# Performance work log

Measured on AMD Instinct MI355X. Metric: run time of the kernel, lower is better.

## Reference

```python
import jax, jax.numpy as jnp
import numpy as np

DIM = 1024
HEADS = 16
DH = DIM // HEADS          # 64
SEQ_LEN = 4096
LATENT = 1024
HIST = SEQ_LEN - LATENT    # 3072
LN_EPS = 1e-5


def setup_inputs() -> dict:
    key = jax.random.key(0)
    ks = jax.random.split(key, 5)
    b = 2
    x = jax.random.normal(ks[0], (b, SEQ_LEN, DIM), dtype=jnp.float32)
    s = 0.02
    Wq = jax.random.normal(ks[1], (DIM, DIM), dtype=jnp.float32) * s
    Wkv = jax.random.normal(ks[2], (DIM, DIM), dtype=jnp.float32) * s
    Wo = jax.random.normal(ks[3], (DIM, DIM), dtype=jnp.float32) * s
    bo = jnp.zeros((DIM,), dtype=jnp.float32)
    gamma = jnp.ones((DH,), dtype=jnp.float32)
    beta = jnp.zeros((DH,), dtype=jnp.float32)
    return {"x": x, "Wq": Wq, "Wkv": Wkv, "Wo": Wo, "bo": bo,
            "gamma": gamma, "beta": beta}


def _rotate_half(t):
    t1, t2 = jnp.split(t, 2, axis=-1)
    return jnp.concatenate([-t2, t1], axis=-1)


def reference(x, Wq, Wkv, Wo, bo, gamma, beta):
    b, n, dim = x.shape
    # projections (nn.Linear: y = x @ W.T), split heads -> (b, h, n, d)
    q = jnp.einsum('bnd,ed->bne', x, Wq).reshape(b, n, HEADS, DH).transpose(0, 2, 1, 3)
    kv = jnp.einsum('bnd,ed->bne', x, Wkv).reshape(b, n, HEADS, DH).transpose(0, 2, 1, 3)

    # layer_num == 0: queries only for the latent segment
    q = q[:, :, HIST:, :]  # (b, h, latent, d)

    # rotary embeddings: concat-style freqs over head dim
    inv_freq = 1.0 / (10000.0 ** (jnp.arange(0, DH, 2, dtype=jnp.float32) / DH))
    freqs = jnp.arange(n, dtype=jnp.float32)[:, None] * inv_freq[None, :]  # (n, DH/2)
    emb = jnp.concatenate([freqs, freqs], axis=-1)  # (n, DH)
    cos, sin = jnp.cos(emb), jnp.sin(emb)
    q = q * cos[HIST:] + _rotate_half(q) * sin[HIST:]
    kv = kv * cos + _rotate_half(kv) * sin

    q = q * (DH ** -0.5)

    # per-kv LayerNorm over head dim
    mu = kv.mean(axis=-1, keepdims=True)
    var = ((kv - mu) ** 2).mean(axis=-1, keepdims=True)
    kvn = (kv - mu) * jax.lax.rsqrt(var + LN_EPS) * gamma + beta

    attn = jnp.einsum('bhid,bhjd->bhij', q, kvn)  # (b, h, latent, n)

    # causal mask only on latent columns: col j (>= HIST) masked if j-HIST > i
    i = jnp.arange(LATENT)[:, None]
    j = jnp.arange(n)[None, :]
    mask = (j - HIST) > i  # false for history columns (j < HIST)
    neg = -jnp.finfo(attn.dtype).max
    attn = jnp.where(mask, neg, attn)

    attn = jax.nn.softmax(attn, axis=-1)
    out = jnp.einsum('bhij,bhjd->bhid', attn, kvn)  # (b, h, latent, d)
    out = out.transpose(0, 2, 1, 3).reshape(b, LATENT, dim)
    return jnp.einsum('bnd,ed->bne', out, Wo) + bo
```

## Files before the change

### kernel.cpp

```cpp
#include <hip/hip_runtime.h>
#include <hip/hip_bf16.h>
#include <cstdint>

#define DIMC 1024
#define HEADS 16
#define DHH 64
#define SEQ 4096
#define LATENT 1024
#define HISTC 3072
#define BATCH 2

typedef __attribute__((ext_vector_type(8))) __bf16 bf16x8;
typedef __attribute__((ext_vector_type(4))) float f32x4;
typedef __attribute__((ext_vector_type(16))) float f32x16;

__global__ void k_convert(const float* __restrict__ in, __bf16* __restrict__ out, int n) {
  int stride = gridDim.x * blockDim.x;
  int nc = n >> 2;
  for (int i = blockIdx.x * blockDim.x + threadIdx.x; i < nc; i += stride) {
    float4 v = reinterpret_cast<const float4*>(in)[i];
    union { __bf16 h[4]; uint64_t u; } p;
    p.h[0] = (__bf16)v.x; p.h[1] = (__bf16)v.y;
    p.h[2] = (__bf16)v.z; p.h[3] = (__bf16)v.w;
    reinterpret_cast<uint64_t*>(out)[i] = p.u;
  }
}

__global__ void k_convert3(const float* __restrict__ a, const float* __restrict__ b,
                           const float* __restrict__ c, __bf16* __restrict__ oa,
                           __bf16* __restrict__ ob, __bf16* __restrict__ oc) {
  int id = blockIdx.x;
  const float* src; __bf16* dst;
  if (id < 512) { src = a; dst = oa; }
  else if (id < 1024) { src = b; dst = ob; id -= 512; }
  else { src = c; dst = oc; id -= 1024; }
#pragma unroll
  for (int k = 0; k < 2; ++k) {
    int idx = id * 512 + k * 256 + threadIdx.x;
    float4 v = reinterpret_cast<const float4*>(src)[idx];
    union { __bf16 h[4]; uint64_t u; } p;
    p.h[0] = (__bf16)v.x; p.h[1] = (__bf16)v.y;
    p.h[2] = (__bf16)v.z; p.h[3] = (__bf16)v.w;
    reinterpret_cast<uint64_t*>(dst)[idx] = p.u;
  }
}

__device__ __forceinline__ void gload16(void* lds, const void* g) {
  __builtin_amdgcn_global_load_lds(
      (const __attribute__((address_space(1))) unsigned int*)g,
      (__attribute__((address_space(3))) unsigned int*)lds, 16, 0, 0);
}

template<int QREMAP, int BIAS>
__launch_bounds__(256)
__global__ void k_gemm(const __bf16* __restrict__ A, const __bf16* __restrict__ Bw,
                       float* __restrict__ C, const float* __restrict__ bias,
                       int M, int N, int K) {
  __shared__ __align__(16) char lds[16384];
  const int t = threadIdx.x;
  const int l = t & 63, w = t >> 6;
  const int wr = w >> 1, wc = w & 1;
  const int m0 = blockIdx.y * 128, n0 = blockIdx.x * 128;
  const int lrow = l & 15, lk = l >> 4;
  f32x4 acc[4][4] = {};

  for (int k0 = 0; k0 < K; k0 += 32) {
    if (k0) __syncthreads();
#pragma unroll
    for (int i = 0; i < 2; ++i) {
      int c = i * 256 + t;
      int row = c >> 2, kc = c & 3;
      int mi = m0 + row;
      if (QREMAP) mi += HISTC + (mi >> 10) * HISTC;
      gload16(lds + c * 16, A + (size_t)mi * K + k0 + kc * 8);
      gload16(lds + 8192 + c * 16, Bw + (size_t)(n0 + row) * K + k0 + kc * 8);
    }
    __syncthreads();
    bf16x8 af[4], bfr[4];
#pragma unroll
    for (int m = 0; m < 4; ++m)
      af[m] = *reinterpret_cast<const bf16x8*>(lds + (wr * 64 + m * 16 + lrow) * 64 + lk * 16);
#pragma unroll
    for (int n = 0; n < 4; ++n)
      bfr[n] = *reinterpret_cast<const bf16x8*>(lds + 8192 + (wc * 64 + n * 16 + lrow) * 64 + lk * 16);
#pragma unroll
    for (int m = 0; m < 4; ++m)
#pragma unroll
      for (int n = 0; n < 4; ++n)
        acc[m][n] = __builtin_amdgcn_mfma_f32_16x16x32_bf16(af[m], bfr[n], acc[m][n], 0, 0, 0);
  }

#pragma unroll
  for (int m = 0; m < 4; ++m)
#pragma unroll
    for (int n = 0; n < 4; ++n)
#pragma unroll
      for (int r = 0; r < 4; ++r) {
        int row = m0 + wr * 64 + m * 16 + (l >> 4) * 4 + r;
        int col = n0 + wc * 64 + n * 16 + (l & 15);
        float v = acc[m][n][r];
        if (BIAS) v += bias[col];
        C[(size_t)row * N + col] = v;
      }
}

__launch_bounds__(256)
__global__ void k_gemmqkv(const __bf16* __restrict__ x16,
                          const __bf16* __restrict__ wkv16,
                          const __bf16* __restrict__ wq16,
                          __bf16* __restrict__ kvn, __bf16* __restrict__ kvnT,
                          __bf16* __restrict__ qb,
                          const float* __restrict__ gamma,
                          const float* __restrict__ beta) {
  __shared__ __align__(16) char lds[16384];
  const int t = threadIdx.x, l = t & 63, w = t >> 6;
  const int wr = w >> 1, wc = w & 1;
  const int by = blockIdx.y;
  const bool isq = by >= 64;
  const int m0 = (isq ? (by - 64) : by) * 128;
  const int n0 = blockIdx.x * 128;
  const __bf16* Bw = isq ? wq16 : wkv16;
  const int lrow = l & 15, lk = l >> 4;
  f32x4 acc[4][4] = {};

  for (int k0 = 0; k0 < 1024; k0 += 32) {
    if (k0) __syncthreads();
#pragma unroll
    for (int i = 0; i < 2; ++i) {
      int c = i * 256 + t;
      int row = c >> 2, kc = c & 3;
      int mi = m0 + row;
      if (isq) mi += HISTC + (mi >> 10) * HISTC;
      gload16(lds + c * 16, x16 + (size_t)mi * 1024 + k0 + kc * 8);
      gload16(lds + 8192 + c * 16, Bw + (size_t)(n0 + row) * 1024 + k0 + kc * 8);
    }
    __syncthreads();
    bf16x8 af[4], bfr[4];
#pragma unroll
    for (int m = 0; m < 4; ++m)
      af[m] = *reinterpret_cast<const bf16x8*>(lds + (wr * 64 + m * 16 + lrow) * 64 + lk * 16);
#pragma unroll
    for (int n = 0; n < 4; ++n)
      bfr[n] = *reinterpret_cast<const bf16x8*>(lds + 8192 + (wc * 64 + n * 16 + lrow) * 64 + lk * 16);
#pragma unroll
    for (int m = 0; m < 4; ++m)
#pragma unroll
      for (int n = 0; n < 4; ++n)
        acc[m][n] = __builtin_amdgcn_mfma_f32_16x16x32_bf16(af[m], bfr[n], acc[m][n], 0, 0, 0);
  }

  const float LG = 0.41524101186f;
  float invf0 = exp2f(-(float)lrow * LG);
  float invf1 = exp2f(-(float)(lrow + 16) * LG);
#pragma unroll
  for (int m = 0; m < 4; ++m)
#pragma unroll
    for (int r = 0; r < 4; ++r) {
      int rl = wr * 64 + m * 16 + lk * 4 + r;
      int pos = isq ? (HISTC + ((m0 + rl) & 1023)) : ((m0 + rl) & 4095);
      float fp = (float)pos;
      float s0, c0, s1, c1;
      sincosf(fp * invf0, &s0, &c0);
      sincosf(fp * invf1, &s1, &c1);
      float a0 = acc[m][0][r], a2 = acc[m][2][r];
      acc[m][0][r] = a0 * c0 - a2 * s0;
      acc[m][2][r] = a2 * c0 + a0 * s0;
      float a1 = acc[m][1][r], a3 = acc[m][3][r];
      acc[m][1][r] = a1 * c1 - a3 * s1;
      acc[m][3][r] = a3 * c1 + a1 * s1;
    }

  const int h = (n0 + wc * 64) >> 6;
  if (!isq) {
    float g4[4], b4[4];
#pragma unroll
    for (int n = 0; n < 4; ++n) { g4[n] = gamma[n * 16 + lrow]; b4[n] = beta[n * 16 + lrow]; }
#pragma unroll
    for (int m = 0; m < 4; ++m)
#pragma unroll
      for (int r = 0; r < 4; ++r) {
        float s1 = acc[m][0][r] + acc[m][1][r] + acc[m][2][r] + acc[m][3][r];
        float s2 = acc[m][0][r] * acc[m][0][r] + acc[m][1][r] * acc[m][1][r] +
                   acc[m][2][r] * acc[m][2][r] + acc[m][3][r] * acc[m][3][r];
#pragma unroll
        for (int mk = 1; mk < 16; mk <<= 1) {
          s1 += __shfl_xor(s1, mk);
          s2 += __shfl_xor(s2, mk);
        }
        float mu = s1 * 0.015625f;
        float var = s2 * 0.015625f - mu * mu;
        float inv = rsqrtf(var + 1e-5f);
#pragma unroll
        for (int n = 0; n < 4; ++n)
          acc[m][n][r] = (acc[m][n][r] - mu) * inv * g4[n] + b4[n];
      }
    const size_t hb = (size_t)((m0 >> 12) * HEADS + h);
#pragma unroll
    for (int m = 0; m < 4; ++m)
#pragma unroll
      for (int r = 0; r < 4; ++r) {
        int pos = (m0 + wr * 64 + m * 16 + lk * 4 + r) & 4095;
#pragma unroll
        for (int n = 0; n < 4; ++n)
          kvn[(hb * SEQ + pos) * DHH + n * 16 + lrow] = (__bf16)acc[m][n][r];
      }
#pragma unroll
    for (int m = 0; m < 4; ++m) {
      int pos0 = (m0 + wr * 64 + m * 16 + lk * 4) & 4095;
      int sp = (pos0 & ~12) | ((pos0 & 4) << 1) | ((pos0 & 8) >> 1);
#pragma unroll
      for (int n = 0; n < 4; ++n) {
        union { __bf16 hh[4]; uint64_t u; } pk;
#pragma unroll
        for (int r = 0; r < 4; ++r) pk.hh[r] = (__bf16)acc[m][n][r];
        *reinterpret_cast<uint64_t*>(kvnT + (hb * DHH + n * 16 + lrow) * SEQ + sp) = pk.u;
      }
    }
  } else {
    const size_t hb = (size_t)((m0 >> 10) * HEADS + h);
#pragma unroll
    for (int m = 0; m < 4; ++m)
#pragma unroll
      for (int r = 0; r < 4; ++r) {
        int qi = (m0 + wr * 64 + m * 16 + lk * 4 + r) & 1023;
#pragma unroll
        for (int n = 0; n < 4; ++n)
          qb[(hb * LATENT + qi) * DHH + n * 16 + lrow] =
              (__bf16)(acc[m][n][r] * 0.18033688011112042f);
      }
  }
}

__device__ __forceinline__ float fexp2(float x) {
#if __has_builtin(__builtin_amdgcn_exp2f)
  return __builtin_amdgcn_exp2f(x);
#else
  return exp2f(x);
#endif
}

__device__ __forceinline__ unsigned pk2(float a, float b) {
  union { __bf16 h[2]; unsigned u; } x;
  x.h[0] = (__bf16)a; x.h[1] = (__bf16)b;
  return x.u;
}

__launch_bounds__(256)
__global__ void k_flash5(const __bf16* __restrict__ qb, const __bf16* __restrict__ kvn,
                         const __bf16* __restrict__ kvnT, __bf16* __restrict__ aout) {
  const int bid = blockIdx.x;
  const int bh = (bid & 7) + 8 * (bid >> 8);
  const int itile = (bid >> 3) & 31;
  const int h = bh & 15, b = bh >> 4;
  const int t = threadIdx.x, l = t & 63, w = t >> 6;
  const int q = l & 31, hi = l >> 5;
  const int iw = itile * 32;
  const int i = iw + q;
  const __bf16* qbase = qb + ((size_t)(b * HEADS + h) * LATENT + iw) * DHH;
  const __bf16* kbase = kvn + (size_t)(b * HEADS + h) * SEQ * DHH;
  const __bf16* vbase = kvnT + (size_t)(b * HEADS + h) * DHH * SEQ;

  __shared__ __align__(16) char smem[4][4352];
  __shared__ float Mlds[4][32];
  __shared__ float Llds[4][32];
  __bf16 (*Vw)[32] = reinterpret_cast<__bf16(*)[32]>(smem[w]);

  bf16x8 qf[4];
#pragma unroll
  for (int c = 0; c < 4; ++c)
    qf[c] = *reinterpret_cast<const bf16x8*>(qbase + (size_t)q * DHH + c * 16 + hi * 8);

  const f32x16 Z = {};
  f32x16 O0 = {}, O1 = {};
  float m_run = -INFINITY, lacc = 0.f;

  const int nt = itile + 97;
  const int t0 = (nt * w) >> 2, t1 = (nt * (w + 1)) >> 2;

  const int srow = l >> 2, scol = l & 3;
  const int wchunk = (scol ^ (srow & 3)) * 8;
  const int sx = q & 3;
  bf16x8 vreg[4], kreg[4];
#pragma unroll
  for (int ii = 0; ii < 4; ++ii)
    vreg[ii] = *reinterpret_cast<const bf16x8*>(
        vbase + (size_t)(ii * 16 + srow) * SEQ + t0 * 32 + scol * 8);
#pragma unroll
  for (int c = 0; c < 4; ++c)
    kreg[c] = *reinterpret_cast<const bf16x8*>(
        kbase + (size_t)(t0 * 32 + q) * DHH + c * 16 + hi * 8);

  for (int tt = t0; tt < t1; ++tt) {
    const int j0 = tt * 32;
    f32x16 S = __builtin_amdgcn_mfma_f32_32x32x16_bf16(kreg[0], qf[0], Z, 0, 0, 0);
#pragma unroll
    for (int c = 1; c < 4; ++c)
      S = __builtin_amdgcn_mfma_f32_32x32x16_bf16(kreg[c], qf[c], S, 0, 0, 0);
#pragma unroll
    for (int ii = 0; ii < 4; ++ii)
      *reinterpret_cast<bf16x8*>(&Vw[ii * 16 + srow][wchunk]) = vreg[ii];
    const int tn = (tt + 1 < t1) ? tt + 1 : tt;
#pragma unroll
    for (int ii = 0; ii < 4; ++ii)
      vreg[ii] = *reinterpret_cast<const bf16x8*>(
          vbase + (size_t)(ii * 16 + srow) * SEQ + tn * 32 + scol * 8);
#pragma unroll
    for (int c = 0; c < 4; ++c)
      kreg[c] = *reinterpret_cast<const bf16x8*>(
          kbase + (size_t)(tn * 32 + q) * DHH + c * 16 + hi * 8);
    if (j0 + 31 > iw + HISTC) {
#pragma unroll
      for (int r = 0; r < 16; ++r) {
        int j = j0 + (r & 3) + 8 * (r >> 2) + 4 * hi;
        if (j > i + HISTC) S[r] = -1e30f;
      }
    }
    float u1 = fmaxf(fmaxf(S[0], S[1]), S[2]);
    float u2 = fmaxf(fmaxf(S[3], S[4]), S[5]);
    float u3 = fmaxf(fmaxf(S[6], S[7]), S[8]);
    float u4 = fmaxf(fmaxf(S[9], S[10]), S[11]);
    float u5 = fmaxf(fmaxf(S[12], S[13]), S[14]);
    float pm = fmaxf(fmaxf(fmaxf(u1, u2), u3), fmaxf(fmaxf(u4, u5), S[15]));
    if (__any(pm > m_run + 8.0f)) {
      pm = fmaxf(pm, __shfl_xor(pm, 32));
      float mn = fmaxf(m_run, pm);
      float sc = fexp2(m_run - mn);
      m_run = mn;
      lacc *= sc;
#pragma unroll
      for (int r = 0; r < 16; ++r) { O0[r] *= sc; O1[r] *= sc; }
    }
    float p[16];
#pragma unroll
    for (int r = 0; r < 16; ++r) p[r] = fexp2(S[r] - m_run);
    float s8[8];
#pragma unroll
    for (int r = 0; r < 8; ++r) s8[r] = p[r] + p[r + 8];
    float s4_0 = s8[0] + s8[4], s4_1 = s8[1] + s8[5];
    float s4_2 = s8[2] + s8[6], s4_3 = s8[3] + s8[7];
    lacc += (s4_0 + s4_1) + (s4_2 + s4_3);
    union { unsigned u[4]; bf16x8 v; } pf0, pf1;
    pf0.u[0] = pk2(p[0], p[1]);   pf0.u[1] = pk2(p[2], p[3]);
    pf0.u[2] = pk2(p[4], p[5]);   pf0.u[3] = pk2(p[6], p[7]);
    pf1.u[0] = pk2(p[8], p[9]);   pf1.u[1] = pk2(p[10], p[11]);
    pf1.u[2] = pk2(p[12], p[13]); pf1.u[3] = pk2(p[14], p[15]);
    {
      bf16x8 va00 = *reinterpret_cast<const bf16x8*>(&Vw[q][(hi ^ sx) * 8]);
      bf16x8 va01 = *reinterpret_cast<const bf16x8*>(&Vw[q][((2 + hi) ^ sx) * 8]);
      bf16x8 va10 = *reinterpret_cast<const bf16x8*>(&Vw[32 + q][(hi ^ sx) * 8]);
      bf16x8 va11 = *reinterpret_cast<const bf16x8*>(&Vw[32 + q][((2 + hi) ^ sx) * 8]);
      O0 = __builtin_amdgcn_mfma_f32_32x32x16_bf16(va00, pf0.v, O0, 0, 0, 0);
      O0 = __builtin_amdgcn_mfma_f32_32x32x16_bf16(va01, pf1.v, O0, 0, 0, 0);
      O1 = __builtin_amdgcn_mfma_f32_32x32x16_bf16(va10, pf0.v, O1, 0, 0, 0);
      O1 = __builtin_amdgcn_mfma_f32_32x32x16_bf16(va11, pf1.v, O1, 0, 0, 0);
    }
  }
  float l_run = lacc + __shfl_xor(lacc, 32);

  float (*Ow)[33] = reinterpret_cast<float(*)[33]>(smem[w]);
  if (hi == 0) { Mlds[w][q] = m_run; Llds[w][q] = l_run; }
#pragma unroll
  for (int r = 0; r < 16; ++r)
    Ow[q][(r & 3) + 8 * (r >> 2) + 4 * hi] = O0[r];
  __syncthreads();
  const int mi = t >> 3, dl = (t & 7) * 4;
  float m0v = Mlds[0][mi], m1v = Mlds[1][mi], m2v = Mlds[2][mi], m3v = Mlds[3][mi];
  float mm = fmaxf(fmaxf(m0v, m1v), fmaxf(m2v, m3v));
  float sc0 = fexp2(m0v - mm), sc1 = fexp2(m1v - mm);
  float sc2 = fexp2(m2v - mm), sc3 = fexp2(m3v - mm);
  float ll = Llds[0][mi] * sc0 + Llds[1][mi] * sc1 + Llds[2][mi] * sc2 + Llds[3][mi] * sc3;
  float inv = 1.f / ll;
  __bf16* orow = aout + ((size_t)(b * LATENT) + iw + mi) * DIMC + h * DHH;
  {
    float(*O0p)[33] = reinterpret_cast<float(*)[33]>(smem[0]);
    float(*O1p)[33] = reinterpret_cast<float(*)[33]>(smem[1]);
    float(*O2p)[33] = reinterpret_cast<float(*)[33]>(smem[2]);
    float(*O3p)[33] = reinterpret_cast<float(*)[33]>(smem[3]);
    union { __bf16 hh[4]; uint2 u2; } pkv;
#pragma unroll
    for (int e = 0; e < 4; ++e) {
      float o = O0p[mi][dl + e] * sc0 + O1p[mi][dl + e] * sc1 +
                O2p[mi][dl + e] * sc2 + O3p[mi][dl + e] * sc3;
      pkv.hh[e] = (__bf16)(o * inv);
    }
    *reinterpret_cast<uint2*>(orow + dl) = pkv.u2;
  }
  __syncthreads();
#pragma unroll
  for (int r = 0; r < 16; ++r)
    Ow[q][(r & 3) + 8 * (r >> 2) + 4 * hi] = O1[r];
  __syncthreads();
  {
    float(*O0p)[33] = reinterpret_cast<float(*)[33]>(smem[0]);
    float(*O1p)[33] = reinterpret_cast<float(*)[33]>(smem[1]);
    float(*O2p)[33] = reinterpret_cast<float(*)[33]>(smem[2]);
    float(*O3p)[33] = reinterpret_cast<float(*)[33]>(smem[3]);
    union { __bf16 hh[4]; uint2 u2; } pkv;
#pragma unroll
    for (int e = 0; e < 4; ++e) {
      float o = O0p[mi][dl + e] * sc0 + O1p[mi][dl + e] * sc1 +
                O2p[mi][dl + e] * sc2 + O3p[mi][dl + e] * sc3;
      pkv.hh[e] = (__bf16)(o * inv);
    }
    *reinterpret_cast<uint2*>(orow + 32 + dl) = pkv.u2;
  }
}

extern "C" void kernel_launch(void* const* d_in, const int* in_sizes, int n_in,
                              void* d_out, int out_size, void* d_ws, size_t ws_size,
                              hipStream_t stream) {
  const float* x = (const float*)d_in[0];
  const float* Wq = (const float*)d_in[1];
  const float* Wkv = (const float*)d_in[2];
  const float* Wo = (const float*)d_in[3];
  const float* bo = (const float*)d_in[4];
  const float* gamma = (const float*)d_in[5];
  const float* beta = (const float*)d_in[6];

  char* ws = (char*)d_ws;
  size_t o = 0;
  __bf16* x16 = (__bf16*)(ws + o);  o += (size_t)BATCH * SEQ * DIMC * 2;
  __bf16* wq16 = (__bf16*)(ws + o); o += (size_t)DIMC * DIMC * 2;
  __bf16* wkv16 = (__bf16*)(ws + o); o += (size_t)DIMC * DIMC * 2;
  __bf16* wo16 = (__bf16*)(ws + o); o += (size_t)DIMC * DIMC * 2;
  __bf16* kvn = (__bf16*)(ws + o);  o += (size_t)BATCH * HEADS * SEQ * DHH * 2;
  __bf16* kvnT = (__bf16*)(ws + o); o += (size_t)BATCH * HEADS * SEQ * DHH * 2;
  __bf16* qb = (__bf16*)(ws + o);   o += (size_t)BATCH * HEADS * LATENT * DHH * 2;
  __bf16* aout = (__bf16*)(ws + o); o += (size_t)BATCH * LATENT * DIMC * 2;

  k_convert<<<2048, 256, 0, stream>>>(x, x16, BATCH * SEQ * DIMC);
  k_convert3<<<1536, 256, 0, stream>>>(Wq, Wkv, Wo, wq16, wkv16, wo16);
  k_gemmqkv<<<dim3(8, 80), 256, 0, stream>>>(x16, wkv16, wq16, kvn, kvnT, qb, gamma, beta);
  k_flash5<<<1024, 256, 0, stream>>>(qb, kvn, kvnT, aout);
  k_gemm<0, 1><<<dim3(8, 16), 256, 0, stream>>>(aout, wo16, (float*)d_out, bo, 2048, 1024, 1024);
}
```

Measured before the change: 173.4 us.

## Load V operands directly from global memory in flash kernel, add MFMA priority hints

Measured after the change: 211.3 us. 21.9% more time.

```diff
diff --git a/kernel.cpp b/kernel.cpp
--- a/kernel.cpp
+++ b/kernel.cpp
@@ -246,7 +246,7 @@
 }
 
 __launch_bounds__(256)
-__global__ void k_flash5(const __bf16* __restrict__ qb, const __bf16* __restrict__ kvn,
+__global__ void k_flash6(const __bf16* __restrict__ qb, const __bf16* __restrict__ kvn,
                          const __bf16* __restrict__ kvnT, __bf16* __restrict__ aout) {
   const int bid = blockIdx.x;
   const int bh = (bid & 7) + 8 * (bid >> 8);
@@ -263,7 +263,6 @@
   __shared__ __align__(16) char smem[4][4352];
   __shared__ float Mlds[4][32];
   __shared__ float Llds[4][32];
-  __bf16 (*Vw)[32] = reinterpret_cast<__bf16(*)[32]>(smem[w]);
 
   bf16x8 qf[4];
 #pragma unroll
@@ -277,37 +276,33 @@
   const int nt = itile + 97;
   const int t0 = (nt * w) >> 2, t1 = (nt * (w + 1)) >> 2;
 
-  const int srow = l >> 2, scol = l & 3;
-  const int wchunk = (scol ^ (srow & 3)) * 8;
-  const int sx = q & 3;
-  bf16x8 vreg[4], kreg[4];
-#pragma unroll
-  for (int ii = 0; ii < 4; ++ii)
-    vreg[ii] = *reinterpret_cast<const bf16x8*>(
-        vbase + (size_t)(ii * 16 + srow) * SEQ + t0 * 32 + scol * 8);
+  const __bf16* kptr = kbase + (size_t)q * DHH + hi * 8;
+  const __bf16* vrow0 = vbase + (size_t)q * SEQ + hi * 8;
+  const __bf16* vrow1 = vbase + (size_t)(32 + q) * SEQ + hi * 8;
+
+  bf16x8 kreg[4];
 #pragma unroll
   for (int c = 0; c < 4; ++c)
-    kreg[c] = *reinterpret_cast<const bf16x8*>(
-        kbase + (size_t)(t0 * 32 + q) * DHH + c * 16 + hi * 8);
+    kreg[c] = *reinterpret_cast<const bf16x8*>(kptr + (size_t)t0 * 32 * DHH + c * 16);
 
   for (int tt = t0; tt < t1; ++tt) {
     const int j0 = tt * 32;
+    bf16x8 va00 = *reinterpret_cast<const bf16x8*>(vrow0 + j0);
+    bf16x8 va01 = *reinterpret_cast<const bf16x8*>(vrow0 + j0 + 16);
+    bf16x8 va10 = *reinterpret_cast<const bf16x8*>(vrow1 + j0);
+    bf16x8 va11 = *reinterpret_cast<const bf16x8*>(vrow1 + j0 + 16);
+    __builtin_amdgcn_s_setprio(1);
     f32x16 S = __builtin_amdgcn_mfma_f32_32x32x16_bf16(kreg[0], qf[0], Z, 0, 0, 0);
-#pragma unroll
-    for (int c = 1; c < 4; ++c)
-      S = __builtin_amdgcn_mfma_f32_32x32x16_bf16(kreg[c], qf[c], S, 0, 0, 0);
-#pragma unroll
-    for (int ii = 0; ii < 4; ++ii)
-      *reinterpret_cast<bf16x8*>(&Vw[ii * 16 + srow][wchunk]) = vreg[ii];
-    const int tn = (tt + 1 < t1) ? tt + 1 : tt;
-#pragma unroll
-    for (int ii = 0; ii < 4; ++ii)
-      vreg[ii] = *reinterpret_cast<const bf16x8*>(
-          vbase + (size_t)(ii * 16 + srow) * SEQ + tn * 32 + scol * 8);
-#pragma unroll
-    for (int c = 0; c < 4; ++c)
-      kreg[c] = *reinterpret_cast<const bf16x8*>(
-          kbase + (size_t)(tn * 32 + q) * DHH + c * 16 + hi * 8);
+    S = __builtin_amdgcn_mfma_f32_32x32x16_bf16(kreg[1], qf[1], S, 0, 0, 0);
+    S = __builtin_amdgcn_mfma_f32_32x32x16_bf16(kreg[2], qf[2], S, 0, 0, 0);
+    S = __builtin_amdgcn_mfma_f32_32x32x16_bf16(kreg[3], qf[3], S, 0, 0, 0);
+    __builtin_amdgcn_s_setprio(0);
+    {
+      const size_t jn = (size_t)((tt + 1 < t1) ? tt + 1 : tt) * 32 * DHH;
+#pragma unroll
+      for (int c = 0; c < 4; ++c)
+        kreg[c] = *reinterpret_cast<const bf16x8*>(kptr + jn + c * 16);
+    }
     if (j0 + 31 > iw + HISTC) {
 #pragma unroll
       for (int r = 0; r < 16; ++r) {
@@ -344,16 +339,12 @@
     pf0.u[2] = pk2(p[4], p[5]);   pf0.u[3] = pk2(p[6], p[7]);
     pf1.u[0] = pk2(p[8], p[9]);   pf1.u[1] = pk2(p[10], p[11]);
     pf1.u[2] = pk2(p[12], p[13]); pf1.u[3] = pk2(p[14], p[15]);
-    {
-      bf16x8 va00 = *reinterpret_cast<const bf16x8*>(&Vw[q][(hi ^ sx) * 8]);
-      bf16x8 va01 = *reinterpret_cast<const bf16x8*>(&Vw[q][((2 + hi) ^ sx) * 8]);
-      bf16x8 va10 = *reinterpret_cast<const bf16x8*>(&Vw[32 + q][(hi ^ sx) * 8]);
-      bf16x8 va11 = *reinterpret_cast<const bf16x8*>(&Vw[32 + q][((2 + hi) ^ sx) * 8]);
-      O0 = __builtin_amdgcn_mfma_f32_32x32x16_bf16(va00, pf0.v, O0, 0, 0, 0);
-      O0 = __builtin_amdgcn_mfma_f32_32x32x16_bf16(va01, pf1.v, O0, 0, 0, 0);
-      O1 = __builtin_amdgcn_mfma_f32_32x32x16_bf16(va10, pf0.v, O1, 0, 0, 0);
-      O1 = __builtin_amdgcn_mfma_f32_32x32x16_bf16(va11, pf1.v, O1, 0, 0, 0);
-    }
+    __builtin_amdgcn_s_setprio(1);
+    O0 = __builtin_amdgcn_mfma_f32_32x32x16_bf16(va00, pf0.v, O0, 0, 0, 0);
+    O0 = __builtin_amdgcn_mfma_f32_32x32x16_bf16(va01, pf1.v, O0, 0, 0, 0);
+    O1 = __builtin_amdgcn_mfma_f32_32x32x16_bf16(va10, pf0.v, O1, 0, 0, 0);
+    O1 = __builtin_amdgcn_mfma_f32_32x32x16_bf16(va11, pf1.v, O1, 0, 0, 0);
+    __builtin_amdgcn_s_setprio(0);
   }
   float l_run = lacc + __shfl_xor(lacc, 32);
 
@@ -431,6 +422,6 @@
   k_convert<<<2048, 256, 0, stream>>>(x, x16, BATCH * SEQ * DIMC);
   k_convert3<<<1536, 256, 0, stream>>>(Wq, Wkv, Wo, wq16, wkv16, wo16);
   k_gemmqkv<<<dim3(8, 80), 256, 0, stream>>>(x16, wkv16, wq16, kvn, kvnT, qb, gamma, beta);
-  k_flash5<<<1024, 256, 0, stream>>>(qb, kvn, kvnT, aout);
+  k_flash6<<<1024, 256, 0, stream>>>(qb, kvn, kvnT, aout);
   k_gemm<0, 1><<<dim3(8, 16), 256, 0, stream>>>(aout, wo16, (float*)d_out, bo, 2048, 1024, 1024);
 }
```
